# Kernel tuning notes

Measured on AMD Instinct MI355X. Metric: run time of the kernel, lower is better.

## Reference

```python
import jax, jax.numpy as jnp
import numpy as np

DIM = 1024
NUM_HEADS = 16
HEAD_DIM = DIM // NUM_HEADS
SCALE = HEAD_DIM ** -0.5


def setup_inputs() -> dict:
    key = jax.random.key(0)
    k_x, k_qkv, k_pw, k_pb = jax.random.split(key, 4)
    B, S = 2, 2048
    x = jax.random.normal(k_x, (B, S, DIM), dtype=jnp.float32)
    # nn.Linear(dim, 3*dim, bias=False): weight [3*dim, dim]
    w_qkv = jax.random.normal(k_qkv, (3 * DIM, DIM), dtype=jnp.float32) * (DIM ** -0.5)
    # nn.Linear(dim, dim): weight [dim, dim], bias [dim]
    w_proj = jax.random.normal(k_pw, (DIM, DIM), dtype=jnp.float32) * (DIM ** -0.5)
    b_proj = jax.random.normal(k_pb, (DIM,), dtype=jnp.float32) * 0.01
    return {"x": x, "w_qkv": w_qkv, "w_proj": w_proj, "b_proj": b_proj}


def reference(x, w_qkv, w_proj, b_proj):
    B, S, D = x.shape
    qkv = jnp.einsum("bsd,ed->bse", x, w_qkv)  # [B,S,3D]
    q, k, v = jnp.split(qkv, 3, axis=-1)
    def heads(t):  # [B,S,D] -> [B,H,S,hd]
        return t.reshape(B, S, NUM_HEADS, HEAD_DIM).transpose(0, 2, 1, 3)
    q, k, v = heads(q), heads(k), heads(v)
    attn = jnp.einsum("bhqd,bhkd->bhqk", q, k) * SCALE  # [B,H,S,S]
    attn = jax.nn.softmax(attn, axis=-1)
    out = jnp.einsum("bhqk,bhkd->bhqd", attn, v)  # [B,H,S,hd]
    out = out.transpose(0, 2, 1, 3).reshape(B, S, D)
    return jnp.einsum("bsd,ed->bse", out, w_proj) + b_proj
```

## Files before the change

kernel.cpp:

```cpp
#include <hip/hip_runtime.h>
#include <stdint.h>

typedef __bf16 bf16;
typedef __bf16 bf16x8 __attribute__((ext_vector_type(8)));
typedef float f32x4 __attribute__((ext_vector_type(4)));
typedef float f32x16 __attribute__((ext_vector_type(16)));

typedef __attribute__((address_space(1))) void gvoid_t;
typedef __attribute__((address_space(3))) void lvoid_t;

__device__ __forceinline__ void gload16(const void* src, void* lds) {
    __builtin_amdgcn_global_load_lds((gvoid_t*)src, (lvoid_t*)lds, 16, 0, 0);
}

__device__ __forceinline__ float fexp2(float x) {
    float r;
    asm("v_exp_f32 %0, %1" : "=v"(r) : "v"(x));
    return r;
}

__global__ __launch_bounds__(256) void cvt_kernel(const float* __restrict__ in,
                                                  bf16* __restrict__ out, int n8) {
    int idx = blockIdx.x * 256 + threadIdx.x;
    int stride = gridDim.x * 256;
    for (int i = idx; i < n8; i += stride) {
        const float4* p = (const float4*)in;
        float4 a = p[(long)i * 2], b = p[(long)i * 2 + 1];
        bf16x8 o;
        o[0] = (bf16)a.x; o[1] = (bf16)a.y; o[2] = (bf16)a.z; o[3] = (bf16)a.w;
        o[4] = (bf16)b.x; o[5] = (bf16)b.y; o[6] = (bf16)b.z; o[7] = (bf16)b.w;
        ((bf16x8*)out)[i] = o;
    }
}

template <bool F32OUT, int BN>
__global__ __launch_bounds__(256) void gemm_bt(const bf16* __restrict__ A,
                                               const bf16* __restrict__ W,
                                               const float* __restrict__ bias,
                                               void* __restrict__ Cout,
                                               const int M, const int N, const int K) {
    constexpr int NT = BN / 32;
    __shared__ __align__(16) bf16 Alds[4096];
    __shared__ __align__(16) bf16 Blds[4096];
    const int t = threadIdx.x;
    const int wid = t >> 6, lane = t & 63;
    const int g = lane >> 4, c = lane & 15;
    const int wm = wid >> 1, wn = wid & 1;
    const long bm = (long)blockIdx.y * 128, bn = (long)blockIdx.x * BN;

    f32x4 acc[4][NT] = {};

    const int arow = t >> 2;
    const int acol = (t & 3) * 8;
    const bf16* Asrc = A + (bm + arow) * (long)K + acol;
    const bf16* Bsrc = W + (bn + arow) * (long)K + acol;
    bf16* adst = Alds + wid * 512;
    bf16* bdst = Blds + wid * 512;

    for (int k0 = 0; k0 < K; k0 += 32) {
        gload16(Asrc + k0, adst);
        gload16(Asrc + k0 + (long)64 * K, adst + 2048);
        gload16(Bsrc + k0, bdst);
        if constexpr (BN == 128)
            gload16(Bsrc + k0 + (long)64 * K, bdst + 2048);
        __syncthreads();
        bf16x8 af[4], bfr[NT];
#pragma unroll
        for (int mt = 0; mt < 4; ++mt)
            af[mt] = *(const bf16x8*)(Alds + (wm * 64 + mt * 16 + c) * 32 + g * 8);
#pragma unroll
        for (int nt = 0; nt < NT; ++nt)
            bfr[nt] = *(const bf16x8*)(Blds + (wn * (BN / 2) + nt * 16 + c) * 32 + g * 8);
#pragma unroll
        for (int mt = 0; mt < 4; ++mt)
#pragma unroll
            for (int nt = 0; nt < NT; ++nt)
                acc[mt][nt] = __builtin_amdgcn_mfma_f32_16x16x32_bf16(af[mt], bfr[nt],
                                                                      acc[mt][nt], 0, 0, 0);
        __syncthreads();
    }
#pragma unroll
    for (int mt = 0; mt < 4; ++mt) {
#pragma unroll
        for (int nt = 0; nt < NT; ++nt) {
#pragma unroll
            for (int i = 0; i < 4; ++i) {
                const long row = bm + wm * 64 + mt * 16 + g * 4 + i;
                const long col = bn + wn * (BN / 2) + nt * 16 + c;
                if constexpr (F32OUT) {
                    ((float*)Cout)[row * N + col] = acc[mt][nt][i] + bias[col];
                } else {
                    ((bf16*)Cout)[row * N + col] = (bf16)acc[mt][nt][i];
                }
            }
        }
    }
}

__global__ __launch_bounds__(256) void vtrans_kernel(const bf16* __restrict__ qkv,
                                                     bf16* __restrict__ Vt) {
    __shared__ float Lf[64 * 65];
    const int t = threadIdx.x;
    const int bid = blockIdx.x;
    const int b = bid >> 9, r = bid & 511;
    const int s0 = (r & 31) * 64, hd0 = (r >> 5) * 64;

    const int sr = t >> 3, scol = (t & 7) * 8;
    const bf16* src = qkv + (long)(b * 2048 + s0 + sr) * 3072 + 2048 + hd0 + scol;
    bf16x8 v0 = *(const bf16x8*)src;
    bf16x8 v1 = *(const bf16x8*)(src + (long)32 * 3072);
#pragma unroll
    for (int e = 0; e < 8; ++e) {
        Lf[(scol + e) * 65 + sr] = (float)v0[e];
        Lf[(scol + e) * 65 + sr + 32] = (float)v1[e];
    }
    __syncthreads();
    const int hr = t >> 2, ss = (t & 3) * 16;
    bf16 outv[16];
#pragma unroll
    for (int j = 0; j < 16; ++j) outv[j] = (bf16)Lf[hr * 65 + ss + j];
    bf16* dst = Vt + ((long)b * 1024 + hd0 + hr) * 2048 + s0 + ss;
    *(bf16x8*)dst = *(bf16x8*)outv;
    *(bf16x8*)(dst + 8) = *(bf16x8*)(outv + 8);
}

__global__ __launch_bounds__(256) void flash_kernel(const bf16* __restrict__ qkv,
                                                    const bf16* __restrict__ Vt,
                                                    bf16* __restrict__ attno) {
    __shared__ __align__(16) bf16 KV[24576];
    __shared__ float LP[128];

    const int t = threadIdx.x;
    const int wid = t >> 6, lane = t & 63;
    const int l31 = lane & 31, hl = lane >> 5;

    const int i0 = blockIdx.x;
    const int xcd = i0 & 7, slot = i0 >> 3;
    const int bh = xcd * 4 + (slot >> 4);
    const int qb = slot & 15;
    const int b = bh >> 4, h = bh & 15;
    const int rowbase = b * 2048;
    const int q0w = qb * 128 + wid * 32;

    bf16x8 qf[4];
    {
        const bf16* qrow = qkv + (long)(rowbase + q0w + l31) * 3072 + h * 64 + hl * 8;
        const float qs = 0.18033688f;
#pragma unroll
        for (int ks = 0; ks < 4; ++ks) {
            bf16x8 a = *(const bf16x8*)(qrow + ks * 16);
#pragma unroll
            for (int e = 0; e < 8; ++e) qf[ks][e] = (bf16)((float)a[e] * qs);
        }
    }

    const int srow = t >> 3, sq = t & 7;
    const int swcol = (sq ^ (srow & 7)) * 8;
    const bf16* ksn = qkv + (long)(rowbase + srow) * 3072 + 1024 + h * 64 + swcol;
    const bf16* vsn = Vt + ((long)b * 1024 + h * 64 + srow) * 2048 + swcol;

    int rdoff[4];
#pragma unroll
    for (int ks = 0; ks < 4; ++ks)
        rdoff[ks] = l31 * 64 + (((ks * 2 + hl) ^ (l31 & 7)) * 8);

    float lpA = 0.f, lpB = 0.f, lpC = 0.f, lpD = 0.f;
    f32x16 oacc0 = {}, oacc1 = {};

    auto stage = [&]() __attribute__((always_inline)) {
    };
    (void)stage;

#define STAGE(BI)                                                        \
    {                                                                    \
        bf16* kd = KV + (BI) * 4096 + wid * 512;                         \
        bf16* vd = KV + 12288 + (BI) * 4096 + wid * 512;                 \
        gload16(ksn, kd);                                                \
        gload16(ksn + 98304, kd + 2048);                                 \
        gload16(vsn, vd);                                                \
        gload16(vsn + 65536, vd + 2048);                                 \
        ksn += 196608;                                                   \
        vsn += 64;                                                       \
    }

    auto compute = [&](int bi) __attribute__((always_inline)) {
        const bf16* Kb = KV + bi * 4096;
        const bf16* Vb = KV + 12288 + bi * 4096;
        f32x16 s0 = {}, s1 = {};
#pragma unroll
        for (int ks = 0; ks < 4; ++ks) {
            bf16x8 kf0 = *(const bf16x8*)(Kb + rdoff[ks]);
            bf16x8 kf1 = *(const bf16x8*)(Kb + 2048 + rdoff[ks]);
            s0 = __builtin_amdgcn_mfma_f32_32x32x16_bf16(kf0, qf[ks], s0, 0, 0, 0);
            s1 = __builtin_amdgcn_mfma_f32_32x32x16_bf16(kf1, qf[ks], s1, 0, 0, 0);
        }
        float p0[16], p1[16];
#pragma unroll
        for (int r = 0; r < 16; ++r) p0[r] = fexp2(s0[r]);
#pragma unroll
        for (int r = 0; r < 16; ++r) p1[r] = fexp2(s1[r]);
#pragma unroll
        for (int r = 0; r < 4; ++r) {
            lpA += p0[r * 4 + 0] + p1[r * 4 + 0];
            lpB += p0[r * 4 + 1] + p1[r * 4 + 1];
            lpC += p0[r * 4 + 2] + p1[r * 4 + 2];
            lpD += p0[r * 4 + 3] + p1[r * 4 + 3];
        }
#pragma unroll
        for (int ks = 0; ks < 4; ++ks) {
            const float* pp = (ks < 2) ? p0 : p1;
            const int s = (ks & 1) * 8;
            unsigned wA, wB, wC, wD;
            asm("v_cvt_pk_bf16_f32 %0, %1, %2" : "=v"(wA) : "v"(pp[s + 0]), "v"(pp[s + 1]));
            asm("v_cvt_pk_bf16_f32 %0, %1, %2" : "=v"(wB) : "v"(pp[s + 4]), "v"(pp[s + 5]));
            asm("v_cvt_pk_bf16_f32 %0, %1, %2" : "=v"(wC) : "v"(pp[s + 2]), "v"(pp[s + 3]));
            asm("v_cvt_pk_bf16_f32 %0, %1, %2" : "=v"(wD) : "v"(pp[s + 6]), "v"(pp[s + 7]));
            asm("v_permlane32_swap_b32 %0, %1" : "+v"(wA), "+v"(wB));
            asm("v_permlane32_swap_b32 %0, %1" : "+v"(wC), "+v"(wD));
            union { unsigned w[4]; bf16x8 v; } pu;
            pu.w[0] = wA; pu.w[1] = wC; pu.w[2] = wB; pu.w[3] = wD;
            bf16x8 vf0 = *(const bf16x8*)(Vb + rdoff[ks]);
            bf16x8 vf1 = *(const bf16x8*)(Vb + 2048 + rdoff[ks]);
            oacc0 = __builtin_amdgcn_mfma_f32_32x32x16_bf16(pu.v, vf0, oacc0, 0, 0, 0);
            oacc1 = __builtin_amdgcn_mfma_f32_32x32x16_bf16(pu.v, vf1, oacc1, 0, 0, 0);
        }
    };

    STAGE(0);
    STAGE(1);

#define FSTEP(CUR, NXT)                                    \
    asm volatile("s_waitcnt vmcnt(4)" ::: "memory");       \
    __builtin_amdgcn_s_barrier();                          \
    STAGE(NXT);                                            \
    compute(CUR);

    for (int t3 = 0; t3 < 10; ++t3) {
        FSTEP(0, 2)
        FSTEP(1, 0)
        FSTEP(2, 1)
    }
    asm volatile("s_waitcnt vmcnt(4)" ::: "memory");
    __builtin_amdgcn_s_barrier();
    compute(0);
    asm volatile("s_waitcnt vmcnt(0)" ::: "memory");
    __builtin_amdgcn_s_barrier();
    compute(1);
#undef FSTEP
#undef STAGE

    float lpart = (lpA + lpB) + (lpC + lpD);
    lpart += __shfl_xor(lpart, 32);
    if (lane < 32) LP[wid * 32 + l31] = lpart;
    float inv[16];
#pragma unroll
    for (int r = 0; r < 16; ++r) {
        const int qrow = (r & 3) + 8 * (r >> 2) + 4 * hl;
        inv[r] = 1.0f / LP[wid * 32 + qrow];
    }

#pragma unroll
    for (int r = 0; r < 16; ++r) {
        const int qrow = (r & 3) + 8 * (r >> 2) + 4 * hl;
        const long rbase = (long)(rowbase + q0w + qrow) * 1024 + h * 64 + l31;
        attno[rbase] = (bf16)(oacc0[r] * inv[r]);
        attno[rbase + 32] = (bf16)(oacc1[r] * inv[r]);
    }
}

extern "C" void kernel_launch(void* const* d_in, const int* in_sizes, int n_in,
                              void* d_out, int out_size, void* d_ws, size_t ws_size,
                              hipStream_t stream) {
    const float* x = (const float*)d_in[0];
    const float* wqkv = (const float*)d_in[1];
    const float* wproj = (const float*)d_in[2];
    const float* bproj = (const float*)d_in[3];

    char* ws = (char*)d_ws;
    bf16* xb     = (bf16*)(ws);
    bf16* Vt     = (bf16*)(ws);
    bf16* wqkvb  = (bf16*)(ws + 8388608);
    bf16* wprojb = (bf16*)(ws + 14680064);
    bf16* qkv    = (bf16*)(ws + 16777216);
    bf16* attno  = (bf16*)(ws + 41943040);
    if (ws_size < 50331648) return;

    cvt_kernel<<<2048, 256, 0, stream>>>(x, xb, 524288);
    cvt_kernel<<<1536, 256, 0, stream>>>(wqkv, wqkvb, 393216);
    cvt_kernel<<<512, 256, 0, stream>>>(wproj, wprojb, 131072);

    gemm_bt<false, 128><<<dim3(24, 32), 256, 0, stream>>>(xb, wqkvb, nullptr, qkv,
                                                          4096, 3072, 1024);

    vtrans_kernel<<<1024, 256, 0, stream>>>(qkv, Vt);

    flash_kernel<<<512, 256, 0, stream>>>(qkv, Vt, attno);

    gemm_bt<true, 64><<<dim3(16, 32), 256, 0, stream>>>(attno, wprojb, bproj, d_out,
                                                        4096, 1024, 1024);
}
```

Before: 129.1 us.

## Merge conversion kernels, relayout flash K/V LDS tiles, add MFMA priority hints

The three fp32-to-bf16 conversion launches become one kernel that branches on the global index, which removes two launch overheads. In the flash kernel the K/V tiles are now staged into LDS in a fragment-ordered layout, so each lane reads contiguous 16-byte chunks at lane*8 instead of XOR-swizzled offsets. s_setprio calls raise wave priority around the MFMA sections. The new LDS layout must exactly match the MFMA operand mapping, and the per-lane global loads now gather from 32 rows per wave, which may coalesce differently.

```diff
diff --git a/kernel.cpp b/kernel.cpp
--- a/kernel.cpp
+++ b/kernel.cpp
@@ -19,17 +19,27 @@
     return r;
 }
 
-__global__ __launch_bounds__(256) void cvt_kernel(const float* __restrict__ in,
-                                                  bf16* __restrict__ out, int n8) {
+__global__ __launch_bounds__(256) void cvt3_kernel(const float* __restrict__ x,
+                                                   const float* __restrict__ wqkv,
+                                                   const float* __restrict__ wproj,
+                                                   bf16* __restrict__ xb,
+                                                   bf16* __restrict__ wqkvb,
+                                                   bf16* __restrict__ wprojb) {
     int idx = blockIdx.x * 256 + threadIdx.x;
     int stride = gridDim.x * 256;
-    for (int i = idx; i < n8; i += stride) {
+    for (int i = idx; i < 1048576; i += stride) {
+        const float* in;
+        bf16* out;
+        int j;
+        if (i < 524288) { in = x; out = xb; j = i; }
+        else if (i < 917504) { in = wqkv; out = wqkvb; j = i - 524288; }
+        else { in = wproj; out = wprojb; j = i - 917504; }
         const float4* p = (const float4*)in;
-        float4 a = p[(long)i * 2], b = p[(long)i * 2 + 1];
+        float4 a = p[(long)j * 2], b = p[(long)j * 2 + 1];
         bf16x8 o;
         o[0] = (bf16)a.x; o[1] = (bf16)a.y; o[2] = (bf16)a.z; o[3] = (bf16)a.w;
         o[4] = (bf16)b.x; o[5] = (bf16)b.y; o[6] = (bf16)b.z; o[7] = (bf16)b.w;
-        ((bf16x8*)out)[i] = o;
+        ((bf16x8*)out)[j] = o;
     }
 }
 
@@ -154,46 +164,43 @@
         }
     }
 
-    const int srow = t >> 3, sq = t & 7;
-    const int swcol = (sq ^ (srow & 7)) * 8;
-    const bf16* ksn = qkv + (long)(rowbase + srow) * 3072 + 1024 + h * 64 + swcol;
-    const bf16* vsn = Vt + ((long)b * 1024 + h * 64 + srow) * 2048 + swcol;
-
-    int rdoff[4];
-#pragma unroll
-    for (int ks = 0; ks < 4; ++ks)
-        rdoff[ks] = l31 * 64 + (((ks * 2 + hl) ^ (l31 & 7)) * 8);
+    const bf16* ksn = qkv + (long)(rowbase + (wid >> 1) * 32 + l31) * 3072 + 1024 + h * 64 +
+                      (wid & 1) * 32 + hl * 8;
+    const bf16* vsn = Vt + ((long)b * 1024 + h * 64 + (wid >> 1) * 32 + l31) * 2048 +
+                      (wid & 1) * 32 + hl * 8;
+    const int kchunk = wid * 1024;
 
     float lpA = 0.f, lpB = 0.f, lpC = 0.f, lpD = 0.f;
     f32x16 oacc0 = {}, oacc1 = {};
 
-    auto stage = [&]() __attribute__((always_inline)) {
-    };
-    (void)stage;
-
 #define STAGE(BI)                                                        \
     {                                                                    \
-        bf16* kd = KV + (BI) * 4096 + wid * 512;                         \
-        bf16* vd = KV + 12288 + (BI) * 4096 + wid * 512;                 \
+        bf16* kd = KV + (BI) * 4096 + kchunk;                            \
+        bf16* vd = KV + 12288 + (BI) * 4096 + kchunk;                    \
         gload16(ksn, kd);                                                \
-        gload16(ksn + 98304, kd + 2048);                                 \
+        gload16(ksn + 16, kd + 512);                                     \
         gload16(vsn, vd);                                                \
-        gload16(vsn + 65536, vd + 2048);                                 \
+        gload16(vsn + 16, vd + 512);                                     \
         ksn += 196608;                                                   \
         vsn += 64;                                                       \
     }
 
+    const bf16* kl;
+    const bf16* vl;
+
     auto compute = [&](int bi) __attribute__((always_inline)) {
-        const bf16* Kb = KV + bi * 4096;
-        const bf16* Vb = KV + 12288 + bi * 4096;
+        kl = KV + bi * 4096 + lane * 8;
+        vl = KV + 12288 + bi * 4096 + lane * 8;
         f32x16 s0 = {}, s1 = {};
+        __builtin_amdgcn_s_setprio(1);
 #pragma unroll
         for (int ks = 0; ks < 4; ++ks) {
-            bf16x8 kf0 = *(const bf16x8*)(Kb + rdoff[ks]);
-            bf16x8 kf1 = *(const bf16x8*)(Kb + 2048 + rdoff[ks]);
+            bf16x8 kf0 = *(const bf16x8*)(kl + ks * 512);
+            bf16x8 kf1 = *(const bf16x8*)(kl + 2048 + ks * 512);
             s0 = __builtin_amdgcn_mfma_f32_32x32x16_bf16(kf0, qf[ks], s0, 0, 0, 0);
             s1 = __builtin_amdgcn_mfma_f32_32x32x16_bf16(kf1, qf[ks], s1, 0, 0, 0);
         }
+        __builtin_amdgcn_s_setprio(0);
         float p0[16], p1[16];
 #pragma unroll
         for (int r = 0; r < 16; ++r) p0[r] = fexp2(s0[r]);
@@ -206,6 +213,7 @@
             lpC += p0[r * 4 + 2] + p1[r * 4 + 2];
             lpD += p0[r * 4 + 3] + p1[r * 4 + 3];
         }
+        __builtin_amdgcn_s_setprio(1);
 #pragma unroll
         for (int ks = 0; ks < 4; ++ks) {
             const float* pp = (ks < 2) ? p0 : p1;
@@ -219,11 +227,12 @@
             asm("v_permlane32_swap_b32 %0, %1" : "+v"(wC), "+v"(wD));
             union { unsigned w[4]; bf16x8 v; } pu;
             pu.w[0] = wA; pu.w[1] = wC; pu.w[2] = wB; pu.w[3] = wD;
-            bf16x8 vf0 = *(const bf16x8*)(Vb + rdoff[ks]);
-            bf16x8 vf1 = *(const bf16x8*)(Vb + 2048 + rdoff[ks]);
+            bf16x8 vf0 = *(const bf16x8*)(vl + ks * 512);
+            bf16x8 vf1 = *(const bf16x8*)(vl + 2048 + ks * 512);
             oacc0 = __builtin_amdgcn_mfma_f32_32x32x16_bf16(pu.v, vf0, oacc0, 0, 0, 0);
             oacc1 = __builtin_amdgcn_mfma_f32_32x32x16_bf16(pu.v, vf1, oacc1, 0, 0, 0);
         }
+        __builtin_amdgcn_s_setprio(0);
     };
 
     STAGE(0);
@@ -285,9 +294,7 @@
     bf16* attno  = (bf16*)(ws + 41943040);
     if (ws_size < 50331648) return;
 
-    cvt_kernel<<<2048, 256, 0, stream>>>(x, xb, 524288);
-    cvt_kernel<<<1536, 256, 0, stream>>>(wqkv, wqkvb, 393216);
-    cvt_kernel<<<512, 256, 0, stream>>>(wproj, wprojb, 131072);
+    cvt3_kernel<<<2048, 256, 0, stream>>>(x, wqkv, wproj, xb, wqkvb, wprojb);
 
     gemm_bt<false, 128><<<dim3(24, 32), 256, 0, stream>>>(xb, wqkvb, nullptr, qkv,
                                                           4096, 3072, 1024);
```

Result: no change. 128.2 us (-0.7%).
